# Performance work log

Measured on AMD Instinct MI355X. Metric: run time of the kernel, lower is better.

The kernel has to match this reference:

```python
import jax, jax.numpy as jnp
import numpy as np

GROUPS = 32
EPS = 1e-5
N_HEADS = 8


def setup_inputs() -> dict:
    key = jax.random.key(0)
    ks = jax.random.split(key, 12)
    B, H, W, C = 16, 64, 64, 512
    Nctx, Dctx = 77, 768
    s_c = 1.0 / np.sqrt(C)
    s_ctx = 1.0 / np.sqrt(Dctx)
    return {
        "x": jax.random.normal(ks[0], (B, H, W, C), jnp.float32),
        "context": jax.random.normal(ks[1], (B, Nctx, Dctx), jnp.float32),
        "gn_scale": jnp.ones((C,), jnp.float32),
        "gn_bias": jnp.zeros((C,), jnp.float32),
        "wq": jax.random.normal(ks[2], (C, C), jnp.float32) * s_c,
        "bq": jnp.zeros((C,), jnp.float32),
        "wk": jax.random.normal(ks[3], (Dctx, C), jnp.float32) * s_ctx,
        "bk": jnp.zeros((C,), jnp.float32),
        "wv": jax.random.normal(ks[4], (Dctx, C), jnp.float32) * s_ctx,
        "bv": jnp.zeros((C,), jnp.float32),
        "wo": jax.random.normal(ks[5], (C, C), jnp.float32) * s_c,
        "bo": jnp.zeros((C,), jnp.float32),
    }


def _group_norm(x, scale, bias):
    B, H, W, C = x.shape
    xg = x.reshape(B, H, W, GROUPS, C // GROUPS)
    mean = jnp.mean(xg, axis=(1, 2, 4), keepdims=True)
    var = jnp.var(xg, axis=(1, 2, 4), keepdims=True)
    xn = (xg - mean) * jax.lax.rsqrt(var + EPS)
    return xn.reshape(B, H, W, C) * scale + bias


def reference(x, context, gn_scale, gn_bias, wq, bq, wk, bk, wv, bv, wo, bo):
    B, H, W, C = x.shape
    head_dim = C // N_HEADS
    h = _group_norm(x, gn_scale, gn_bias)
    h_flat = h.reshape(B, H * W, C)
    Q = h_flat @ wq + bq                      # [B, N, C]
    K = context @ wk + bk                     # [B, Nctx, C]
    V = context @ wv + bv

    def split_heads(t):
        b, n, c = t.shape
        return t.reshape(b, n, N_HEADS, head_dim).transpose(0, 2, 1, 3)

    Qh, Kh, Vh = split_heads(Q), split_heads(K), split_heads(V)
    scale = 1.0 / jnp.sqrt(jnp.asarray(head_dim, x.dtype))
    scores = jnp.einsum('bhid,bhjd->bhij', Qh, Kh) * scale
    attn = jax.nn.softmax(scores, axis=-1)
    out = jnp.einsum('bhij,bhjd->bhid', attn, Vh)  # [B, h, N, d]
    out = out.transpose(0, 2, 1, 3).reshape(B, H * W, C)
    out = out @ wo + bo
    return out.reshape(B, H, W, C) + x
```

## Files before the change

kernel.cpp:

```cpp
#include <hip/hip_runtime.h>
#include <hip/hip_bf16.h>

typedef __attribute__((ext_vector_type(4))) float f32x4;
typedef __attribute__((ext_vector_type(8))) short bf16x8;
typedef unsigned short u16;

#define AS1 __attribute__((address_space(1)))
#define AS3 __attribute__((address_space(3)))

#define B_    16
#define HW_   4096
#define C_    512
#define NCTX  77
#define DCTX  768
#define NH    8
#define HD    64
#define EPSV  1e-5f

__device__ inline u16 f2bf(float f) {
    union { float f; unsigned u; } v; v.f = f;
    unsigned r = v.u + 0x7fffu + ((v.u >> 16) & 1u);
    return (u16)(r >> 16);
}

__global__ __launch_bounds__(256) void gn_trans(const float* __restrict__ x,
                                                float* __restrict__ mean,
                                                float* __restrict__ rstd,
                                                const float* __restrict__ wq,
                                                const float* __restrict__ wk,
                                                const float* __restrict__ wv,
                                                const float* __restrict__ wo,
                                                u16* __restrict__ wqT,
                                                u16* __restrict__ wkT,
                                                u16* __restrict__ wvT,
                                                u16* __restrict__ woT) {
    if (blockIdx.x < 512) {
        int b = blockIdx.x >> 5, g = blockIdx.x & 31;
        const float* px = x + (size_t)b * HW_ * C_ + g * 16;
        float s = 0.f, ss = 0.f;
        for (int t = threadIdx.x; t < HW_ * 4; t += 256) {
            int hw = t >> 2, c4 = (t & 3) * 4;
            const float4 v = *(const float4*)(px + (size_t)hw * C_ + c4);
            s  += v.x + v.y + v.z + v.w;
            ss += v.x * v.x + v.y * v.y + v.z * v.z + v.w * v.w;
        }
        for (int off = 32; off; off >>= 1) { s += __shfl_xor(s, off); ss += __shfl_xor(ss, off); }
        __shared__ float red[2][4];
        int wv_ = threadIdx.x >> 6, lane = threadIdx.x & 63;
        if (lane == 0) { red[0][wv_] = s; red[1][wv_] = ss; }
        __syncthreads();
        if (threadIdx.x == 0) {
            float S = red[0][0] + red[0][1] + red[0][2] + red[0][3];
            float SS = red[1][0] + red[1][1] + red[1][2] + red[1][3];
            float mn = S / 65536.f;
            float var = SS / 65536.f - mn * mn;
            mean[blockIdx.x] = mn;
            rstd[blockIdx.x] = rsqrtf(var + EPSV);
        }
    } else {
        int idx = (blockIdx.x - 512) * 256 + threadIdx.x;
        if (idx < 262144) {
            int k = idx >> 9, n = idx & 511;
            wqT[(size_t)n * 512 + k] = f2bf(wq[idx]);
        } else if (idx < 655360) {
            int i = idx - 262144;
            int k = i >> 9, n = i & 511;
            wkT[(size_t)n * 768 + k] = f2bf(wk[i]);
        } else if (idx < 1048576) {
            int i = idx - 655360;
            int k = i >> 9, n = i & 511;
            wvT[(size_t)n * 768 + k] = f2bf(wv[i]);
        } else if (idx < 1310720) {
            int i = idx - 1048576;
            int k = i >> 9, n = i & 511;
            woT[(size_t)n * 512 + k] = f2bf(wo[i]);
        }
    }
}

__global__ __launch_bounds__(256, 2) void gemm_fusedq(const float* __restrict__ x,
                                                      const float* __restrict__ mean,
                                                      const float* __restrict__ rstd,
                                                      const float* __restrict__ gns,
                                                      const float* __restrict__ gnb,
                                                      const u16* __restrict__ Bt,
                                                      const float* __restrict__ bias,
                                                      u16* __restrict__ out,
                                                      const float* __restrict__ ctx,
                                                      const u16* __restrict__ wkT,
                                                      const u16* __restrict__ wvT,
                                                      const float* __restrict__ bk,
                                                      const float* __restrict__ bv,
                                                      u16* __restrict__ kb,
                                                      u16* __restrict__ vb) {
    __shared__ __align__(16) u16 POOL[32768];
    int tid = threadIdx.x, lane = tid & 63, wid = tid >> 6;
    int q = lane >> 4, r16 = lane & 15;

    if (blockIdx.x >= 2048) {
        constexpr int M = 1232, K = 768;
        u16 (*As)[40] = (u16(*)[40])&POOL[0];
        u16 (*Bs)[40] = (u16(*)[40])&POOL[5120];
        int idx = blockIdx.x - 2048;
        int bx = idx & 7, byk = idx >> 3;
        const u16* Btl = (bx < 4) ? wkT : wvT;
        const float* bi = (bx < 4) ? bk : bv;
        u16* o = (bx < 4) ? kb : vb;
        int wm = wid >> 1, wn = wid & 1;
        int row0 = byk * 128, col0 = (bx & 3) * 128;

        f32x4 acc[4][4];
#pragma unroll
        for (int i = 0; i < 4; i++)
#pragma unroll
            for (int j = 0; j < 4; j++) acc[i][j] = (f32x4){0.f, 0.f, 0.f, 0.f};

        for (int k0 = 0; k0 < K; k0 += 32) {
#pragma unroll
            for (int it = 0; it < 2; ++it) {
                int e = it * 256 + tid;
                int rr = e >> 2, kc = (e & 3) * 8;
                int ga = row0 + rr; if (ga > M - 1) ga = M - 1;
                float4 a0 = *(const float4*)(ctx + (size_t)ga * K + k0 + kc);
                float4 a1 = *(const float4*)(ctx + (size_t)ga * K + k0 + kc + 4);
                bf16x8 av;
                av[0] = (short)f2bf(a0.x); av[1] = (short)f2bf(a0.y);
                av[2] = (short)f2bf(a0.z); av[3] = (short)f2bf(a0.w);
                av[4] = (short)f2bf(a1.x); av[5] = (short)f2bf(a1.y);
                av[6] = (short)f2bf(a1.z); av[7] = (short)f2bf(a1.w);
                *(bf16x8*)&As[rr][kc] = av;
                int gb = col0 + rr;
                bf16x8 bv8 = *(const bf16x8*)(Btl + (size_t)gb * K + k0 + kc);
                *(bf16x8*)&Bs[rr][kc] = bv8;
            }
            __syncthreads();
            bf16x8 afr[4], bfr[4];
#pragma unroll
            for (int mi = 0; mi < 4; mi++) afr[mi] = *(const bf16x8*)&As[wm * 64 + mi * 16 + r16][q * 8];
#pragma unroll
            for (int ni = 0; ni < 4; ni++) bfr[ni] = *(const bf16x8*)&Bs[wn * 64 + ni * 16 + r16][q * 8];
#pragma unroll
            for (int mi = 0; mi < 4; mi++)
#pragma unroll
                for (int ni = 0; ni < 4; ni++)
                    acc[mi][ni] = __builtin_amdgcn_mfma_f32_16x16x32_bf16(afr[mi], bfr[ni], acc[mi][ni], 0, 0, 0);
            __syncthreads();
        }

#pragma unroll
        for (int mi = 0; mi < 4; mi++) {
#pragma unroll
            for (int rr = 0; rr < 4; rr++) {
                int grow = row0 + wm * 64 + mi * 16 + q * 4 + rr;
                if (grow >= M) continue;
#pragma unroll
                for (int ni = 0; ni < 4; ni++) {
                    int gcol = col0 + wn * 64 + ni * 16 + r16;
                    float v = acc[mi][ni][rr] + bi[gcol];
                    o[(size_t)grow * 512 + gcol] = f2bf(v);
                }
            }
        }
        return;
    }

    constexpr int K = 512;
    u16 (*LA)[8192] = (u16(*)[8192])&POOL[0];
    u16 (*LB)[8192] = (u16(*)[8192])&POOL[16384];
    int wr = wid >> 1, wc = wid & 1;

    int orig = blockIdx.x;
    int wg = (orig & 7) * 256 + (orig >> 3);
    int bx = wg & 3, by = wg >> 2;
    int row0 = by * 128, col0 = bx * 128;

    int srow = tid >> 3;
    int schunk = (tid & 7) ^ (srow & 7);
    const u16* gB = Bt + (size_t)(col0 + srow) * K + schunk * 8;
    const int lo = tid * 8;

    int c8 = tid & 7;
    int rbase = (tid >> 3) * 4;
    const float* xb = x + (size_t)(row0 + rbase) * 512 + c8 * 8;
    int bg0 = (row0 >> 12) * 32;

    f32x4 acc[4][4];
#pragma unroll
    for (int i = 0; i < 4; i++)
#pragma unroll
        for (int j = 0; j < 4; j++) acc[i][j] = (f32x4){0.f, 0.f, 0.f, 0.f};

    float4 ar[8];
    float mn, rs;
    float4 s0v, s1v, b0v, b1v;

#define LOADA(kt) do { _Pragma("unroll")                                          \
    for (int i_ = 0; i_ < 4; ++i_) {                                              \
        ar[2 * i_]     = *(const float4*)(xb + (kt) * 64 + (size_t)i_ * 512);     \
        ar[2 * i_ + 1] = *(const float4*)(xb + (kt) * 64 + (size_t)i_ * 512 + 4); \
    } } while (0)

#define LOADP(kt) do { int c0_ = (kt) * 64 + c8 * 8; int bg_ = bg0 + (c0_ >> 4);  \
    mn = mean[bg_]; rs = rstd[bg_];                                               \
    s0v = *(const float4*)(gns + c0_); s1v = *(const float4*)(gns + c0_ + 4);     \
    b0v = *(const float4*)(gnb + c0_); b1v = *(const float4*)(gnb + c0_ + 4);     \
  } while (0)

#define WRITEA(nbuf) do {                                                         \
    float m2_[8], a2_[8];                                                         \
    m2_[0]=rs*s0v.x; m2_[1]=rs*s0v.y; m2_[2]=rs*s0v.z; m2_[3]=rs*s0v.w;           \
    m2_[4]=rs*s1v.x; m2_[5]=rs*s1v.y; m2_[6]=rs*s1v.z; m2_[7]=rs*s1v.w;           \
    a2_[0]=b0v.x-mn*m2_[0]; a2_[1]=b0v.y-mn*m2_[1];                               \
    a2_[2]=b0v.z-mn*m2_[2]; a2_[3]=b0v.w-mn*m2_[3];                               \
    a2_[4]=b1v.x-mn*m2_[4]; a2_[5]=b1v.y-mn*m2_[5];                               \
    a2_[6]=b1v.z-mn*m2_[6]; a2_[7]=b1v.w-mn*m2_[7];                               \
    _Pragma("unroll")                                                             \
    for (int i_ = 0; i_ < 4; ++i_) {                                              \
        int row_ = rbase + i_;                                                    \
        bf16x8 pk_;                                                               \
        pk_[0]=(short)f2bf(ar[2*i_].x  *m2_[0]+a2_[0]);                           \
        pk_[1]=(short)f2bf(ar[2*i_].y  *m2_[1]+a2_[1]);                           \
        pk_[2]=(short)f2bf(ar[2*i_].z  *m2_[2]+a2_[2]);                           \
        pk_[3]=(short)f2bf(ar[2*i_].w  *m2_[3]+a2_[3]);                           \
        pk_[4]=(short)f2bf(ar[2*i_+1].x*m2_[4]+a2_[4]);                           \
        pk_[5]=(short)f2bf(ar[2*i_+1].y*m2_[5]+a2_[5]);                           \
        pk_[6]=(short)f2bf(ar[2*i_+1].z*m2_[6]+a2_[6]);                           \
        pk_[7]=(short)f2bf(ar[2*i_+1].w*m2_[7]+a2_[7]);                           \
        *(bf16x8*)&LA[nbuf][row_ * 64 + ((c8 ^ (row_ & 7)) * 8)] = pk_;           \
    } } while (0)

#define STG_B(kt, s) __builtin_amdgcn_global_load_lds( \
        (const AS1 void*)(gB + (kt) * 64 + (size_t)((s) * 32) * K), \
        (AS3 void*)(&LB[(kt) & 1][(s) * 2048 + lo]), 16, 0, 0)

#define PHASE_(buf, h, ks) do {                                                            \
    bf16x8 afr[2], bfr[4];                                                                 \
    const int ch_ = (((ks) * 4 + q) ^ (r16 & 7)) * 8;                                      \
    _Pragma("unroll")                                                                      \
    for (int mi = 0; mi < 2; mi++)                                                         \
        afr[mi] = *(const bf16x8*)&LA[buf][(wr * 64 + ((h) * 2 + mi) * 16 + r16) * 64 + ch_]; \
    _Pragma("unroll")                                                                      \
    for (int ni = 0; ni < 4; ni++)                                                         \
        bfr[ni] = *(const bf16x8*)&LB[buf][(wc * 64 + ni * 16 + r16) * 64 + ch_];          \
    __builtin_amdgcn_s_setprio(1);                                                         \
    _Pragma("unroll")                                                                      \
    for (int mi = 0; mi < 2; mi++)                                                         \
      _Pragma("unroll")                                                                    \
      for (int ni = 0; ni < 4; ni++)                                                       \
        acc[(h) * 2 + mi][ni] =                                                            \
            __builtin_amdgcn_mfma_f32_16x16x32_bf16(afr[mi], bfr[ni], acc[(h) * 2 + mi][ni], 0, 0, 0); \
    __builtin_amdgcn_s_setprio(0);                                                         \
  } while (0)

    LOADA(0); LOADP(0);
    asm volatile("" ::: "memory");
    STG_B(0, 0); STG_B(0, 1); STG_B(0, 2); STG_B(0, 3);
    asm volatile("s_waitcnt vmcnt(4)" ::: "memory");
    WRITEA(0);
    asm volatile("s_waitcnt lgkmcnt(0)" ::: "memory");

#pragma unroll
    for (int t = 0; t < 7; ++t) {
        const int buf = t & 1;
        LOADA(t + 1); LOADP(t + 1);
        asm volatile("" ::: "memory");
        STG_B(t + 1, 0); STG_B(t + 1, 1); STG_B(t + 1, 2); STG_B(t + 1, 3);
        asm volatile("s_waitcnt vmcnt(18)" ::: "memory");
        __builtin_amdgcn_s_barrier();
        asm volatile("" ::: "memory");
        PHASE_(buf, 0, 0); PHASE_(buf, 1, 0); PHASE_(buf, 0, 1); PHASE_(buf, 1, 1);
        asm volatile("s_waitcnt vmcnt(4)" ::: "memory");
        WRITEA(buf ^ 1);
        asm volatile("s_waitcnt lgkmcnt(0)" ::: "memory");
        __builtin_amdgcn_s_barrier();
        asm volatile("" ::: "memory");
    }
    asm volatile("s_waitcnt vmcnt(0) lgkmcnt(0)" ::: "memory");
    __builtin_amdgcn_s_barrier();
    asm volatile("" ::: "memory");
    PHASE_(1, 0, 0); PHASE_(1, 1, 0); PHASE_(1, 0, 1); PHASE_(1, 1, 1);
#undef LOADA
#undef LOADP
#undef WRITEA
#undef STG_B
#undef PHASE_

#pragma unroll
    for (int mi = 0; mi < 4; mi++) {
#pragma unroll
        for (int rr = 0; rr < 4; rr++) {
            int grow = row0 + wr * 64 + mi * 16 + q * 4 + rr;
#pragma unroll
            for (int ni = 0; ni < 4; ni++) {
                int gcol = col0 + wc * 64 + ni * 16 + r16;
                float v = acc[mi][ni][rr] + bias[gcol];
                out[(size_t)grow * 512 + gcol] = f2bf(v);
            }
        }
    }
}

__global__ __launch_bounds__(256, 4) void gemm_ring(const u16* __restrict__ A,
                                                    const u16* __restrict__ Bt,
                                                    const float* __restrict__ bias,
                                                    const float* __restrict__ res,
                                                    float* __restrict__ out) {
    constexpr int K = 512;
    __shared__ __align__(16) u16 LA[2][4096];
    __shared__ __align__(16) u16 LB[2][4096];
    int tid = threadIdx.x, lane = tid & 63, wid = tid >> 6;
    int wr = wid >> 1, wc = wid & 1;
    int q = lane >> 4, r16 = lane & 15;

    int orig = blockIdx.x;
    int wg = (orig & 7) * 256 + (orig >> 3);
    int bx = wg & 3, by = wg >> 2;
    int row0 = by * 128, col0 = bx * 128;

    int srow = tid >> 2;
    int schunk = (tid & 3) ^ (srow & 3);
    const u16* gA = A + (size_t)(row0 + srow) * K + schunk * 8;
    const u16* gB = Bt + (size_t)(col0 + srow) * K + schunk * 8;
    const int lo = tid * 8;

    f32x4 acc[4][4];
#pragma unroll
    for (int i = 0; i < 4; i++)
#pragma unroll
        for (int j = 0; j < 4; j++) acc[i][j] = (f32x4){0.f, 0.f, 0.f, 0.f};

#define STG(kt) do { int sl_ = (kt) & 1;                                              \
    __builtin_amdgcn_global_load_lds((const AS1 void*)(gA + (kt) * 32),               \
                                     (AS3 void*)(&LA[sl_][lo]), 16, 0, 0);            \
    __builtin_amdgcn_global_load_lds((const AS1 void*)(gA + (kt) * 32 + (size_t)64 * K), \
                                     (AS3 void*)(&LA[sl_][2048 + lo]), 16, 0, 0);     \
    __builtin_amdgcn_global_load_lds((const AS1 void*)(gB + (kt) * 32),               \
                                     (AS3 void*)(&LB[sl_][lo]), 16, 0, 0);            \
    __builtin_amdgcn_global_load_lds((const AS1 void*)(gB + (kt) * 32 + (size_t)64 * K), \
                                     (AS3 void*)(&LB[sl_][2048 + lo]), 16, 0, 0);     \
  } while (0)

#define COMPUTE(sl) do {                                                              \
    bf16x8 afr[4], bfr[4];                                                            \
    const int ch_ = (q ^ (r16 & 3)) * 8;                                              \
    _Pragma("unroll")                                                                 \
    for (int mi = 0; mi < 4; mi++)                                                    \
        afr[mi] = *(const bf16x8*)&LA[sl][(wr * 64 + mi * 16 + r16) * 32 + ch_];      \
    _Pragma("unroll")                                                                 \
    for (int ni = 0; ni < 4; ni++)                                                    \
        bfr[ni] = *(const bf16x8*)&LB[sl][(wc * 64 + ni * 16 + r16) * 32 + ch_];      \
    __builtin_amdgcn_s_setprio(1);                                                    \
    _Pragma("unroll")                                                                 \
    for (int mi = 0; mi < 4; mi++)                                                    \
      _Pragma("unroll")                                                               \
      for (int ni = 0; ni < 4; ni++)                                                  \
        acc[mi][ni] = __builtin_amdgcn_mfma_f32_16x16x32_bf16(afr[mi], bfr[ni], acc[mi][ni], 0, 0, 0); \
    __builtin_amdgcn_s_setprio(0);                                                    \
  } while (0)

    STG(0);
#pragma unroll
    for (int t = 0; t < 15; ++t) {
        STG(t + 1);
        asm volatile("s_waitcnt vmcnt(4)" ::: "memory");
        asm volatile("s_barrier" ::: "memory");
        COMPUTE(t & 1);
        asm volatile("s_barrier" ::: "memory");
    }
    asm volatile("s_waitcnt vmcnt(0)" ::: "memory");
    asm volatile("s_barrier" ::: "memory");
    COMPUTE(1);
#undef STG
#undef COMPUTE

#pragma unroll
    for (int mi = 0; mi < 4; mi++) {
#pragma unroll
        for (int rr = 0; rr < 4; rr++) {
            int grow = row0 + wr * 64 + mi * 16 + q * 4 + rr;
#pragma unroll
            for (int ni = 0; ni < 4; ni++) {
                int gcol = col0 + wc * 64 + ni * 16 + r16;
                float v = acc[mi][ni][rr] + bias[gcol];
                size_t idx = (size_t)grow * 512 + gcol;
                out[idx] = v + res[idx];
            }
        }
    }
}

__global__ __launch_bounds__(256) void attn_mfma(const u16* __restrict__ Qb,
                                                 const u16* __restrict__ Kb,
                                                 const u16* __restrict__ Vb,
                                                 u16* __restrict__ Ob) {
    __shared__ __align__(16) u16 Ks[80][72];
    __shared__ __align__(16) u16 VT[64][104];
    __shared__ __align__(16) u16 Ps[64][104];
    int tid = threadIdx.x, lane = tid & 63, wv = tid >> 6;
    int q = lane >> 4, r16 = lane & 15;
    int tile0 = blockIdx.x * 8;
    int bh = blockIdx.y;
    int b = bh >> 3, h = bh & 7;

    {
        unsigned* p0 = (unsigned*)&Ks[0][0];
        for (int i = tid; i < 2880; i += 256) p0[i] = 0u;
        unsigned* p1 = (unsigned*)&VT[0][0];
        for (int i = tid; i < 3328; i += 256) p1[i] = 0u;
        unsigned* p2 = (unsigned*)&Ps[0][0];
        for (int i = tid; i < 3328; i += 256) p2[i] = 0u;
    }
    __syncthreads();

    size_t kvbase = ((size_t)b * NCTX) * C_ + h * HD;
    for (int c = tid; c < NCTX * 8; c += 256) {
        int j = c >> 3, d8 = (c & 7) * 8;
        *(bf16x8*)&Ks[j][d8] = *(const bf16x8*)(Kb + kvbase + (size_t)j * C_ + d8);
    }
    for (int t = tid; t < NCTX * 64; t += 256) {
        int j = t >> 6, d = t & 63;
        VT[d][j] = Vb[kvbase + (size_t)j * C_ + d];
    }
    __syncthreads();

    const size_t tstep = (size_t)64 * C_;
    const u16* qp = Qb + ((size_t)b * HW_ + wv * 16 + r16) * C_ + h * HD + q * 8;
    bool v4 = (r16 < NCTX - 64);

    bf16x8 qc0 = *(const bf16x8*)(qp + (size_t)tile0 * tstep);
    bf16x8 qc1 = *(const bf16x8*)(qp + (size_t)tile0 * tstep + 32);

    for (int it = 0; it < 8; ++it) {
        int tile = tile0 + it;
        bf16x8 qn0 = qc0, qn1 = qc1;
        if (it < 7) {
            qn0 = *(const bf16x8*)(qp + (size_t)(tile + 1) * tstep);
            qn1 = *(const bf16x8*)(qp + (size_t)(tile + 1) * tstep + 32);
        }

        f32x4 accs[5];
#pragma unroll
        for (int nt = 0; nt < 5; ++nt) accs[nt] = (f32x4){0.f, 0.f, 0.f, 0.f};
#pragma unroll
        for (int nt = 0; nt < 5; ++nt) {
            bf16x8 kf = *(const bf16x8*)&Ks[nt * 16 + r16][q * 8];
            accs[nt] = __builtin_amdgcn_mfma_f32_16x16x32_bf16(qc0, kf, accs[nt], 0, 0, 0);
        }
#pragma unroll
        for (int nt = 0; nt < 5; ++nt) {
            bf16x8 kf = *(const bf16x8*)&Ks[nt * 16 + r16][32 + q * 8];
            accs[nt] = __builtin_amdgcn_mfma_f32_16x16x32_bf16(qc1, kf, accs[nt], 0, 0, 0);
        }

#pragma unroll
        for (int r = 0; r < 4; ++r) {
            float s[5];
#pragma unroll
            for (int nt = 0; nt < 5; ++nt) s[nt] = accs[nt][r] * 0.125f;
            float m = fmaxf(fmaxf(fmaxf(s[0], s[1]), fmaxf(s[2], s[3])), v4 ? s[4] : -3.0e38f);
#pragma unroll
            for (int off = 1; off < 16; off <<= 1) m = fmaxf(m, __shfl_xor(m, off));
            float e[5], sum = 0.f;
#pragma unroll
            for (int nt = 0; nt < 5; ++nt) {
                e[nt] = (nt < 4 || v4) ? __expf(s[nt] - m) : 0.f;
                sum += e[nt];
            }
#pragma unroll
            for (int off = 1; off < 16; off <<= 1) sum += __shfl_xor(sum, off);
            float inv = 1.0f / sum;
            int prow = wv * 16 + q * 4 + r;
#pragma unroll
            for (int nt = 0; nt < 5; ++nt)
                Ps[prow][nt * 16 + r16] = f2bf(e[nt] * inv);
        }

        f32x4 acco[4];
#pragma unroll
        for (int nt = 0; nt < 4; ++nt) acco[nt] = (f32x4){0.f, 0.f, 0.f, 0.f};
#pragma unroll
        for (int ks = 0; ks < 3; ++ks) {
            bf16x8 pf = *(const bf16x8*)&Ps[wv * 16 + r16][ks * 32 + q * 8];
#pragma unroll
            for (int nt = 0; nt < 4; ++nt) {
                bf16x8 vf = *(const bf16x8*)&VT[nt * 16 + r16][ks * 32 + q * 8];
                acco[nt] = __builtin_amdgcn_mfma_f32_16x16x32_bf16(pf, vf, acco[nt], 0, 0, 0);
            }
        }

        int row0 = tile * 64 + wv * 16;
#pragma unroll
        for (int nt = 0; nt < 4; ++nt)
#pragma unroll
            for (int r = 0; r < 4; ++r) {
                int row = row0 + q * 4 + r;
                int col = h * HD + nt * 16 + r16;
                Ob[((size_t)b * HW_ + row) * C_ + col] = f2bf(acco[nt][r]);
            }
        qc0 = qn0; qc1 = qn1;
    }
}

extern "C" void kernel_launch(void* const* d_in, const int* in_sizes, int n_in,
                              void* d_out, int out_size, void* d_ws, size_t ws_size,
                              hipStream_t stream) {
    const float* x   = (const float*)d_in[0];
    const float* ctx = (const float*)d_in[1];
    const float* gns = (const float*)d_in[2];
    const float* gnb = (const float*)d_in[3];
    const float* wq  = (const float*)d_in[4];
    const float* bq  = (const float*)d_in[5];
    const float* wk  = (const float*)d_in[6];
    const float* bk  = (const float*)d_in[7];
    const float* wv  = (const float*)d_in[8];
    const float* bv  = (const float*)d_in[9];
    const float* wo  = (const float*)d_in[10];
    const float* bo  = (const float*)d_in[11];

    char* ws = (char*)d_ws;
    float* mean = (float*)(ws + 0);
    float* rstd = (float*)(ws + 2048);
    u16* wqT  = (u16*)(ws + 4096);
    u16* wkT  = (u16*)(ws + 528384);
    u16* wvT  = (u16*)(ws + 1314816);
    u16* woT  = (u16*)(ws + 2101248);
    u16* aob  = (u16*)(ws + 4517888);
    u16* qb   = (u16*)(ws + 71626752);
    u16* kb   = (u16*)(ws + 138735616);
    u16* vb   = (u16*)(ws + 139997184);

    gn_trans<<<5632, 256, 0, stream>>>(x, mean, rstd, wq, wk, wv, wo, wqT, wkT, wvT, woT);

    gemm_fusedq<<<2128, 256, 0, stream>>>(x, mean, rstd, gns, gnb, wqT, bq, qb,
                                          ctx, wkT, wvT, bk, bv, kb, vb);

    attn_mfma<<<dim3(8, 128), 256, 0, stream>>>(qb, kb, vb, aob);

    gemm_ring<<<2048, 256, 0, stream>>>(aob, woT, bo, x, (float*)d_out);
}
```

Baseline: 281.6 us.

## Halve K-tile in fused GroupNorm+Q GEMM to fit four blocks per CU

The fused GroupNorm + Q-projection GEMM drops its K tile from 64 to 32. This halves LDS use to 32 KB and lets launch bounds request four blocks per CU instead of two. The A/B staging, swizzle, waitcnt thresholds and loop count (16 iterations) are reworked to match. The intent is higher occupancy to hide global and LDS latency, at the cost of twice as many barriers and iterations and smaller per-stage prefetch. The K/V branch shares the smaller pool and must still fit in 32 KB.

Result: slower. 372.0 us (+32.1%).

```diff
diff --git a/kernel.cpp b/kernel.cpp
--- a/kernel.cpp
+++ b/kernel.cpp
@@ -78,7 +78,7 @@
     }
 }
 
-__global__ __launch_bounds__(256, 2) void gemm_fusedq(const float* __restrict__ x,
+__global__ __launch_bounds__(256, 4) void gemm_fusedq(const float* __restrict__ x,
                                                       const float* __restrict__ mean,
                                                       const float* __restrict__ rstd,
                                                       const float* __restrict__ gns,
@@ -93,7 +93,7 @@
                                                       const float* __restrict__ bv,
                                                       u16* __restrict__ kb,
                                                       u16* __restrict__ vb) {
-    __shared__ __align__(16) u16 POOL[32768];
+    __shared__ __align__(16) u16 POOL[16384];
     int tid = threadIdx.x, lane = tid & 63, wid = tid >> 6;
     int q = lane >> 4, r16 = lane & 15;
 
@@ -165,8 +165,8 @@
     }
 
     constexpr int K = 512;
-    u16 (*LA)[8192] = (u16(*)[8192])&POOL[0];
-    u16 (*LB)[8192] = (u16(*)[8192])&POOL[16384];
+    u16* LA = &POOL[0];
+    u16* LB = &POOL[8192];
     int wr = wid >> 1, wc = wid & 1;
 
     int orig = blockIdx.x;
@@ -174,14 +174,14 @@
     int bx = wg & 3, by = wg >> 2;
     int row0 = by * 128, col0 = bx * 128;
 
-    int srow = tid >> 3;
-    int schunk = (tid & 7) ^ (srow & 7);
-    const u16* gB = Bt + (size_t)(col0 + srow) * K + schunk * 8;
+    int srB = tid >> 2;
+    int cB = (tid & 3) ^ (srB & 3);
+    const u16* gB = Bt + (size_t)(col0 + srB) * K + cB * 8;
     const int lo = tid * 8;
 
-    int c8 = tid & 7;
-    int rbase = (tid >> 3) * 4;
-    const float* xb = x + (size_t)(row0 + rbase) * 512 + c8 * 8;
+    int c4 = tid & 3;
+    int r0l = (tid >> 2) * 2;
+    const float* xb = x + (size_t)(row0 + r0l) * 512 + c4 * 8;
     int bg0 = (row0 >> 12) * 32;
 
     f32x4 acc[4][4];
@@ -190,86 +190,87 @@
 #pragma unroll
         for (int j = 0; j < 4; j++) acc[i][j] = (f32x4){0.f, 0.f, 0.f, 0.f};
 
-    float4 ar[8];
+    float4 ar0, ar1, ar2, ar3;
     float mn, rs;
     float4 s0v, s1v, b0v, b1v;
 
-#define LOADA(kt) do { _Pragma("unroll")                                          \
-    for (int i_ = 0; i_ < 4; ++i_) {                                              \
-        ar[2 * i_]     = *(const float4*)(xb + (kt) * 64 + (size_t)i_ * 512);     \
-        ar[2 * i_ + 1] = *(const float4*)(xb + (kt) * 64 + (size_t)i_ * 512 + 4); \
-    } } while (0)
-
-#define LOADP(kt) do { int c0_ = (kt) * 64 + c8 * 8; int bg_ = bg0 + (c0_ >> 4);  \
+#define LOADA(kt) do {                                      \
+    ar0 = *(const float4*)(xb + (kt) * 32);                 \
+    ar1 = *(const float4*)(xb + (kt) * 32 + 4);             \
+    ar2 = *(const float4*)(xb + (kt) * 32 + 512);           \
+    ar3 = *(const float4*)(xb + (kt) * 32 + 516);           \
+  } while (0)
+
+#define LOADP(kt) do { int c0_ = (kt) * 32 + c4 * 8; int bg_ = bg0 + (c0_ >> 4);  \
     mn = mean[bg_]; rs = rstd[bg_];                                               \
     s0v = *(const float4*)(gns + c0_); s1v = *(const float4*)(gns + c0_ + 4);     \
     b0v = *(const float4*)(gnb + c0_); b1v = *(const float4*)(gnb + c0_ + 4);     \
   } while (0)
 
 #define WRITEA(nbuf) do {                                                         \
-    float m2_[8], a2_[8];                                                         \
-    m2_[0]=rs*s0v.x; m2_[1]=rs*s0v.y; m2_[2]=rs*s0v.z; m2_[3]=rs*s0v.w;           \
-    m2_[4]=rs*s1v.x; m2_[5]=rs*s1v.y; m2_[6]=rs*s1v.z; m2_[7]=rs*s1v.w;           \
-    a2_[0]=b0v.x-mn*m2_[0]; a2_[1]=b0v.y-mn*m2_[1];                               \
-    a2_[2]=b0v.z-mn*m2_[2]; a2_[3]=b0v.w-mn*m2_[3];                               \
-    a2_[4]=b1v.x-mn*m2_[4]; a2_[5]=b1v.y-mn*m2_[5];                               \
-    a2_[6]=b1v.z-mn*m2_[6]; a2_[7]=b1v.w-mn*m2_[7];                               \
-    _Pragma("unroll")                                                             \
-    for (int i_ = 0; i_ < 4; ++i_) {                                              \
-        int row_ = rbase + i_;                                                    \
-        bf16x8 pk_;                                                               \
-        pk_[0]=(short)f2bf(ar[2*i_].x  *m2_[0]+a2_[0]);                           \
-        pk_[1]=(short)f2bf(ar[2*i_].y  *m2_[1]+a2_[1]);                           \
-        pk_[2]=(short)f2bf(ar[2*i_].z  *m2_[2]+a2_[2]);                           \
-        pk_[3]=(short)f2bf(ar[2*i_].w  *m2_[3]+a2_[3]);                           \
-        pk_[4]=(short)f2bf(ar[2*i_+1].x*m2_[4]+a2_[4]);                           \
-        pk_[5]=(short)f2bf(ar[2*i_+1].y*m2_[5]+a2_[5]);                           \
-        pk_[6]=(short)f2bf(ar[2*i_+1].z*m2_[6]+a2_[6]);                           \
-        pk_[7]=(short)f2bf(ar[2*i_+1].w*m2_[7]+a2_[7]);                           \
-        *(bf16x8*)&LA[nbuf][row_ * 64 + ((c8 ^ (row_ & 7)) * 8)] = pk_;           \
-    } } while (0)
-
-#define STG_B(kt, s) __builtin_amdgcn_global_load_lds( \
-        (const AS1 void*)(gB + (kt) * 64 + (size_t)((s) * 32) * K), \
-        (AS3 void*)(&LB[(kt) & 1][(s) * 2048 + lo]), 16, 0, 0)
-
-#define PHASE_(buf, h, ks) do {                                                            \
-    bf16x8 afr[2], bfr[4];                                                                 \
-    const int ch_ = (((ks) * 4 + q) ^ (r16 & 7)) * 8;                                      \
-    _Pragma("unroll")                                                                      \
-    for (int mi = 0; mi < 2; mi++)                                                         \
-        afr[mi] = *(const bf16x8*)&LA[buf][(wr * 64 + ((h) * 2 + mi) * 16 + r16) * 64 + ch_]; \
-    _Pragma("unroll")                                                                      \
-    for (int ni = 0; ni < 4; ni++)                                                         \
-        bfr[ni] = *(const bf16x8*)&LB[buf][(wc * 64 + ni * 16 + r16) * 64 + ch_];          \
-    __builtin_amdgcn_s_setprio(1);                                                         \
-    _Pragma("unroll")                                                                      \
-    for (int mi = 0; mi < 2; mi++)                                                         \
-      _Pragma("unroll")                                                                    \
-      for (int ni = 0; ni < 4; ni++)                                                       \
-        acc[(h) * 2 + mi][ni] =                                                            \
-            __builtin_amdgcn_mfma_f32_16x16x32_bf16(afr[mi], bfr[ni], acc[(h) * 2 + mi][ni], 0, 0, 0); \
-    __builtin_amdgcn_s_setprio(0);                                                         \
+    float m_[8], a_[8];                                                           \
+    m_[0]=rs*s0v.x; m_[1]=rs*s0v.y; m_[2]=rs*s0v.z; m_[3]=rs*s0v.w;               \
+    m_[4]=rs*s1v.x; m_[5]=rs*s1v.y; m_[6]=rs*s1v.z; m_[7]=rs*s1v.w;               \
+    a_[0]=b0v.x-mn*m_[0]; a_[1]=b0v.y-mn*m_[1];                                   \
+    a_[2]=b0v.z-mn*m_[2]; a_[3]=b0v.w-mn*m_[3];                                   \
+    a_[4]=b1v.x-mn*m_[4]; a_[5]=b1v.y-mn*m_[5];                                   \
+    a_[6]=b1v.z-mn*m_[6]; a_[7]=b1v.w-mn*m_[7];                                   \
+    bf16x8 p0_, p1_;                                                              \
+    p0_[0]=(short)f2bf(ar0.x*m_[0]+a_[0]); p0_[1]=(short)f2bf(ar0.y*m_[1]+a_[1]); \
+    p0_[2]=(short)f2bf(ar0.z*m_[2]+a_[2]); p0_[3]=(short)f2bf(ar0.w*m_[3]+a_[3]); \
+    p0_[4]=(short)f2bf(ar1.x*m_[4]+a_[4]); p0_[5]=(short)f2bf(ar1.y*m_[5]+a_[5]); \
+    p0_[6]=(short)f2bf(ar1.z*m_[6]+a_[6]); p0_[7]=(short)f2bf(ar1.w*m_[7]+a_[7]); \
+    p1_[0]=(short)f2bf(ar2.x*m_[0]+a_[0]); p1_[1]=(short)f2bf(ar2.y*m_[1]+a_[1]); \
+    p1_[2]=(short)f2bf(ar2.z*m_[2]+a_[2]); p1_[3]=(short)f2bf(ar2.w*m_[3]+a_[3]); \
+    p1_[4]=(short)f2bf(ar3.x*m_[4]+a_[4]); p1_[5]=(short)f2bf(ar3.y*m_[5]+a_[5]); \
+    p1_[6]=(short)f2bf(ar3.z*m_[6]+a_[6]); p1_[7]=(short)f2bf(ar3.w*m_[7]+a_[7]); \
+    *(bf16x8*)&LA[(nbuf) * 4096 + r0l * 32 + ((c4 ^ (r0l & 3)) * 8)] = p0_;       \
+    *(bf16x8*)&LA[(nbuf) * 4096 + (r0l + 1) * 32 + ((c4 ^ ((r0l + 1) & 3)) * 8)] = p1_; \
+  } while (0)
+
+#define STG_B(kt) do { int sl_ = ((kt) & 1) * 4096;                                    \
+    __builtin_amdgcn_global_load_lds((const AS1 void*)(gB + (kt) * 32),                \
+                                     (AS3 void*)(&LB[sl_ + lo]), 16, 0, 0);            \
+    __builtin_amdgcn_global_load_lds((const AS1 void*)(gB + (kt) * 32 + (size_t)64 * K), \
+                                     (AS3 void*)(&LB[sl_ + 2048 + lo]), 16, 0, 0);     \
+  } while (0)
+
+#define COMPUTE(sl) do {                                                               \
+    bf16x8 afr[4], bfr[4];                                                             \
+    const int ch_ = (q ^ (r16 & 3)) * 8;                                               \
+    _Pragma("unroll")                                                                  \
+    for (int mi = 0; mi < 4; mi++)                                                     \
+        afr[mi] = *(const bf16x8*)&LA[(sl) * 4096 + (wr * 64 + mi * 16 + r16) * 32 + ch_]; \
+    _Pragma("unroll")                                                                  \
+    for (int ni = 0; ni < 4; ni++)                                                     \
+        bfr[ni] = *(const bf16x8*)&LB[(sl) * 4096 + (wc * 64 + ni * 16 + r16) * 32 + ch_]; \
+    __builtin_amdgcn_s_setprio(1);                                                     \
+    _Pragma("unroll")                                                                  \
+    for (int mi = 0; mi < 4; mi++)                                                     \
+      _Pragma("unroll")                                                                \
+      for (int ni = 0; ni < 4; ni++)                                                   \
+        acc[mi][ni] = __builtin_amdgcn_mfma_f32_16x16x32_bf16(afr[mi], bfr[ni], acc[mi][ni], 0, 0, 0); \
+    __builtin_amdgcn_s_setprio(0);                                                     \
   } while (0)
 
     LOADA(0); LOADP(0);
     asm volatile("" ::: "memory");
-    STG_B(0, 0); STG_B(0, 1); STG_B(0, 2); STG_B(0, 3);
-    asm volatile("s_waitcnt vmcnt(4)" ::: "memory");
+    STG_B(0);
+    asm volatile("s_waitcnt vmcnt(2)" ::: "memory");
     WRITEA(0);
     asm volatile("s_waitcnt lgkmcnt(0)" ::: "memory");
 
 #pragma unroll
-    for (int t = 0; t < 7; ++t) {
+    for (int t = 0; t < 15; ++t) {
         const int buf = t & 1;
         LOADA(t + 1); LOADP(t + 1);
         asm volatile("" ::: "memory");
-        STG_B(t + 1, 0); STG_B(t + 1, 1); STG_B(t + 1, 2); STG_B(t + 1, 3);
-        asm volatile("s_waitcnt vmcnt(18)" ::: "memory");
+        STG_B(t + 1);
+        asm volatile("s_waitcnt vmcnt(12)" ::: "memory");
         __builtin_amdgcn_s_barrier();
         asm volatile("" ::: "memory");
-        PHASE_(buf, 0, 0); PHASE_(buf, 1, 0); PHASE_(buf, 0, 1); PHASE_(buf, 1, 1);
-        asm volatile("s_waitcnt vmcnt(4)" ::: "memory");
+        COMPUTE(buf);
+        asm volatile("s_waitcnt vmcnt(2)" ::: "memory");
         WRITEA(buf ^ 1);
         asm volatile("s_waitcnt lgkmcnt(0)" ::: "memory");
         __builtin_amdgcn_s_barrier();
@@ -278,12 +279,12 @@
     asm volatile("s_waitcnt vmcnt(0) lgkmcnt(0)" ::: "memory");
     __builtin_amdgcn_s_barrier();
     asm volatile("" ::: "memory");
-    PHASE_(1, 0, 0); PHASE_(1, 1, 0); PHASE_(1, 0, 1); PHASE_(1, 1, 1);
+    COMPUTE(1);
 #undef LOADA
 #undef LOADP
 #undef WRITEA
 #undef STG_B
-#undef PHASE_
+#undef COMPUTE
 
 #pragma unroll
     for (int mi = 0; mi < 4; mi++) {
```
